# Kernel tuning notes

Hardware: AMD Instinct MI355X
Metric: run time of the kernel (lower is better)

Reference implementation:

```python
import jax, jax.numpy as jnp
import numpy as np

HID = 4544; NH = 71; NKV = 1; HD = 64  # Falcon-7B MQA geometry (head_dim hardcoded 64 in _split_heads)
B = 1; U = 32; C = 4; S = 2048          # batch, users, kv chunks, chunk length


def rotate_half(x):
    d = x.shape[-1] // 2
    return jnp.concatenate((-x[..., d:], x[..., :d]), axis=-1)


def setup_inputs() -> dict:
    key = jax.random.key(0)
    ks = jax.random.split(key, 7)
    hidden_states = jax.random.normal(ks[0], (B, U, HID), jnp.float32)
    cos = jax.random.uniform(ks[1], (1, U, 1, HD), jnp.float32, -1.0, 1.0)
    sin = jax.random.uniform(ks[2], (1, U, 1, HD), jnp.float32, -1.0, 1.0)
    k_cache = jax.random.normal(ks[3], (C, B, U, S, HD), jnp.float32)
    v_cache = jax.random.normal(ks[4], (C, B, U, S, HD), jnp.float32)
    attn_masks = jnp.zeros((C, B, U, S), jnp.float32)
    w_qkv = jax.random.normal(ks[5], ((NKV * (NH // NKV + 2)) * HD, HID), jnp.float32) * 0.02
    w_dense = jax.random.normal(ks[6], (HID, HID), jnp.float32) * 0.02
    return {"hidden_states": hidden_states, "cos": cos, "sin": sin,
            "k_cache": k_cache, "v_cache": v_cache, "attn_masks": attn_masks,
            "w_qkv": w_qkv, "w_dense": w_dense}


def reference(hidden_states, cos, sin, k_cache, v_cache, attn_masks, w_qkv, w_dense):
    b, u, _ = hidden_states.shape
    # fused QKV projection (Linear without bias: x @ W.T)
    fused = hidden_states @ w_qkv.T                      # [b,u,(NH+2*NKV)*HD]
    qkv = fused.reshape(b, u, NKV, NH // NKV + 2, HD)    # _split_heads view
    q = qkv[:, :, :, :-2].reshape(b, u, NH, HD)          # query heads
    k_cur = qkv[:, :, :, -2].reshape(b, u, NKV, HD)      # shared MQA key head
    v_cur = qkv[:, :, :, -1].reshape(b, u, NKV, HD)      # shared MQA value head
    # rotary embedding (apply_rotary_pos_emb)
    q = q * cos + rotate_half(q) * sin
    k_cur = k_cur * cos + rotate_half(k_cur) * sin
    inv = 1.0 / jnp.sqrt(jnp.float32(HD))
    # flash-decode over cached chunks: scores [c,b,u,n,s]
    scores = jnp.einsum('bund,cbusd->cbuns', q, k_cache) * inv
    scores = scores + attn_masks[:, :, :, None, :]
    m_c = jnp.max(scores, axis=-1, keepdims=True)        # [c,b,u,n,1] local max
    p = jnp.exp(scores - m_c)
    l_c = jnp.sum(p, axis=-1, keepdims=True)             # local row sums
    # current token = length-1 chunk (its local max is itself, local sum is 1)
    s_cur = jnp.einsum('bund,bued->bune', q, k_cur) * inv  # [b,u,n,1]
    g = jnp.maximum(jnp.max(m_c, axis=0), s_cur)           # global max [b,u,n,1]
    factor = jnp.exp(m_c - g[None])                        # per-chunk rescale
    out = jnp.einsum('cbuns,cbusd->bund', factor * p, v_cache)
    cur_w = jnp.exp(s_cur - g)                             # [b,u,n,1]
    out = out + cur_w * v_cur                              # v_cur broadcasts over heads
    scale = jnp.sum(factor * l_c, axis=0) + cur_w
    out = out / scale
    attn = out.reshape(b, u, NH * HD)
    return attn @ w_dense.T
```

## Files before the change

kernel.cpp:

```cpp
#include <hip/hip_runtime.h>
#include <hip/hip_bf16.h>

typedef __bf16 bf16_t;
typedef __bf16 bf16x8 __attribute__((ext_vector_type(8)));
typedef float  f32x4  __attribute__((ext_vector_type(4)));

#define MFMA16(A,B,C) __builtin_amdgcn_mfma_f32_16x16x32_bf16(A,B,C,0,0,0)

constexpr int HIDc = 4544;
constexpr int NHc  = 71;
constexpr int NHPc = 80;
constexpr int HDc  = 64;
constexpr int Uc   = 32;
constexpr int Sc   = 2048;
constexpr int RQ   = 4672;

constexpr size_t OFF_FUSED = 0;
constexpr size_t OFF_QHI   = 598016;
constexpr size_t OFF_QLO   = 925696;
constexpr size_t OFF_KCUR  = 1253376;
constexpr size_t OFF_VCUR  = 1261568;
constexpr size_t OFF_MP    = 1269760;
constexpr size_t OFF_LP    = 1415168;
constexpr size_t OFF_AHI   = 1560576;
constexpr size_t OFF_ALO   = 1851392;
constexpr size_t OFF_OP    = 2142208;

__device__ __forceinline__ bf16x8 ld8f(const float* base, long eidx) {
  const float* p = base + eidx;
  const f32x4 a = *(const f32x4*)p;
  const f32x4 b = *(const f32x4*)(p + 4);
  bf16x8 r;
  r[0]=(bf16_t)a[0]; r[1]=(bf16_t)a[1]; r[2]=(bf16_t)a[2]; r[3]=(bf16_t)a[3];
  r[4]=(bf16_t)b[0]; r[5]=(bf16_t)b[1]; r[6]=(bf16_t)b[2]; r[7]=(bf16_t)b[3];
  return r;
}

__device__ __forceinline__ void cp16(const float* g, float* l) {
  __builtin_amdgcn_global_load_lds((const __attribute__((address_space(1))) void*)g,
                                   (__attribute__((address_space(3))) void*)l, 16, 0, 0);
}
__device__ __forceinline__ void cp4(const float* g, float* l) {
  __builtin_amdgcn_global_load_lds((const __attribute__((address_space(1))) void*)g,
                                   (__attribute__((address_space(3))) void*)l, 4, 0, 0);
}

__global__ __launch_bounds__(256) void k_zeros(float* fused, float* out) {
  const int i = blockIdx.x*256 + threadIdx.x;
  if (i < Uc*RQ) fused[i] = 0.f;
  else           out[i - Uc*RQ] = 0.f;
}

__global__ __launch_bounds__(256) void k_qkv(
    const float* __restrict__ hidden, const float* __restrict__ wqkv,
    float* __restrict__ fused)
{
  const int h = blockIdx.x, y = blockIdx.y;
  const int t = threadIdx.x;
  const int wave = t >> 6, lane = t & 63;
  const int c = lane & 15, q4 = lane >> 4;
  const int mt = wave & 1, kh = wave >> 1;
  const int ks0 = y*18;
  const int ksn = min(18, 142 - ks0);
  const int h1  = ksn >> 1;
  const int kbeg = ks0 + (kh ? h1 : 0);
  const int kend = ks0 + (kh ? ksn : h1);
  __shared__ float sD[Uc*HDc];

  const long abase = (long)(mt*16 + c)*HIDc + q4*8;
  const long bbase = ((long)h*64 + c)*HIDc + q4*8;
  f32x4 acc[4] = {};
#pragma unroll 3
  for (int ks = kbeg; ks < kend; ++ks) {
    const bf16x8 af = ld8f(hidden, abase + ks*32);
#pragma unroll
    for (int nf = 0; nf < 4; ++nf) {
      const bf16x8 bv = ld8f(wqkv, bbase + (long)nf*16*HIDc + ks*32);
      acc[nf] = MFMA16(af, bv, acc[nf]);
    }
  }
  if (kh == 0) {
#pragma unroll
    for (int r = 0; r < 4; ++r)
#pragma unroll
      for (int nf = 0; nf < 4; ++nf)
        sD[(mt*16 + q4*4 + r)*64 + nf*16 + c] = acc[nf][r];
  }
  __syncthreads();
  if (kh == 1) {
#pragma unroll
    for (int r = 0; r < 4; ++r)
#pragma unroll
      for (int nf = 0; nf < 4; ++nf)
        sD[(mt*16 + q4*4 + r)*64 + nf*16 + c] += acc[nf][r];
  }
  __syncthreads();
  for (int i = t; i < Uc*HDc; i += 256)
    atomicAdd(&fused[(long)(i >> 6)*RQ + h*64 + (i & 63)], sD[i]);
}

__global__ __launch_bounds__(256) void k_rotary(
    const float* __restrict__ fused,
    const float* __restrict__ cosp, const float* __restrict__ sinp,
    bf16_t* __restrict__ qhi, bf16_t* __restrict__ qlo,
    float* __restrict__ kcur, float* __restrict__ vcur)
{
  const int h  = blockIdx.x;
  const int u0 = blockIdx.y*8;
  const int t = threadIdx.x;
  __shared__ float sD[8*HDc];
  if (h < 73) {
    for (int i = t; i < 8*HDc; i += 256)
      sD[i] = fused[(long)(u0 + (i >> 6))*RQ + h*64 + (i & 63)];
    __syncthreads();
  }
  if (h >= NHc) {
    for (int i = t; i < 8*HDc; i += 256) {
      const long idx = (((long)(u0 + (i >> 6)))*NHPc + h)*HDc + (i & 63);
      qhi[idx] = (bf16_t)0.f;  qlo[idx] = (bf16_t)0.f;
    }
  }
  if (h >= 73) return;
  for (int i = t; i < 8*HDc; i += 256) {
    const int u = u0 + (i >> 6), d = i & 63;
    const float x = sD[i];
    const float partner = sD[i ^ 32];
    const float cs = cosp[u*HDc + d];
    const float sn = sinp[u*HDc + d];
    const float rh = (d < 32) ? -partner : partner;
    const float val = x*cs + rh*sn;
    if (h < NHc) {
      const long idx = ((long)u*NHPc + h)*HDc + d;
      const bf16_t hi = (bf16_t)val;
      qhi[idx] = hi;
      qlo[idx] = (bf16_t)(val - (float)hi);
    } else if (h == NHc) {
      kcur[u*HDc + d] = val;
    } else {
      vcur[u*HDc + d] = x;
    }
  }
}

constexpr int ATTN_SLOT_F   = 4096;
constexpr int ATTN_STAGE_F  = 4*ATTN_SLOT_F;
constexpr int ATTN_SMEM_F   = ATTN_STAGE_F + 2048;
constexpr int ATTN_SMEM_BYTES = ATTN_SMEM_F * 4;

__global__ __launch_bounds__(512, 4) void k_attn(
    const float* __restrict__ kc, const float* __restrict__ vc,
    const float* __restrict__ masks,
    const bf16_t* __restrict__ qhi, const bf16_t* __restrict__ qlo,
    float* __restrict__ Mp, float* __restrict__ Lp, float* __restrict__ Op,
    const int NPB)
{
  extern __shared__ float smem[];
  const int u  = blockIdx.x;
  const int pb = blockIdx.y;
  const int tid = threadIdx.x;
  const int wave = __builtin_amdgcn_readfirstlane(tid >> 6);
  const int lane = tid & 63;
  const int c    = lane & 15;
  const int q4   = lane >> 4;
  const int pbpc = NPB >> 2;
  const int keys_pb = 2048 / pbpc;
  const int ph_cnt  = keys_pb >> 6;
  const int chunk = pb / pbpc;
  const int inner = pb - chunk*pbpc;
  const int s_base = inner*keys_pb;
  const long kvbase = ((long)(chunk*Uc + u))*Sc;

  float* const stage = smem;
  float* const smask = smem + ATTN_STAGE_F;

  const int srow = lane >> 4;
  const int scol = (lane & 15) << 2;

  if (wave >= 5) {
    if (wave == 7) {
      const int nmc = keys_pb >> 6;
      const float* gM = masks + kvbase + s_base;
      for (int i = 0; i < nmc; ++i)
        cp4(gM + i*64 + lane, smask + i*64);
      for (int p = 0; p < ph_cnt; ++p) {
        __builtin_amdgcn_s_barrier();
        if (p == 0) asm volatile("s_waitcnt vmcnt(0)" ::: "memory");
        __builtin_amdgcn_s_barrier();
      }
      return;
    }
    const float* gsrc = (wave == 5) ? kc : vc;
    const int vofs = (wave == 6) ? 2048 : 0;
#pragma unroll
    for (int sl = 0; sl < 2; ++sl) {
      const long tb = (kvbase + s_base + sl*32) * 64;
      float* dst = stage + sl*ATTN_SLOT_F + vofs;
#pragma unroll
      for (int i = 0; i < 8; ++i) {
        const int row = i*4 + srow;
        const int fz = ((row & 7) << 2) ^ (((row >> 3) & 1) << 4);
        cp16(gsrc + tb + row*64 + (scol ^ fz), dst + i*256);
      }
    }
    for (int p = 0; p < ph_cnt; ++p) {
      __builtin_amdgcn_s_barrier();
      if (p + 1 < ph_cnt) {
        const int g = ((p+1) & 1)*2;
#pragma unroll
        for (int sl = 0; sl < 2; ++sl) {
          const long tb = (kvbase + s_base + (long)(p+1)*64 + sl*32) * 64;
          float* dst = stage + (g + sl)*ATTN_SLOT_F + vofs;
#pragma unroll
          for (int i = 0; i < 8; ++i) {
            const int row = i*4 + srow;
            const int fz = ((row & 7) << 2) ^ (((row >> 3) & 1) << 4);
            cp16(gsrc + tb + row*64 + (scol ^ fz), dst + i*256);
          }
        }
        asm volatile("s_waitcnt vmcnt(16)" ::: "memory");
      } else {
        asm volatile("s_waitcnt vmcnt(0)" ::: "memory");
      }
      __builtin_amdgcn_s_barrier();
    }
    return;
  }

  const int ht = wave;
  bf16x8 qh[2], ql[2];
  {
    const bf16_t* qb  = qhi + ((long)u*NHPc + ht*16 + c)*HDc + q4*8;
    const bf16_t* qb2 = qlo + ((long)u*NHPc + ht*16 + c)*HDc + q4*8;
#pragma unroll
    for (int ks = 0; ks < 2; ++ks) {
      qh[ks] = *(const bf16x8*)(qb  + ks*32);
      ql[ks] = *(const bf16x8*)(qb2 + ks*32);
    }
  }

  float m_i = -INFINITY, l_i = 0.f;
  f32x4 Oa[4] = {};

  const int krow0 = ((c >> 2) << 3) + (c & 3);

  for (int p = 0; p < ph_cnt; ++p) {
    __syncthreads();
    __syncthreads();
    const int g = (p & 1)*2;

    f32x4 S[2][2];
    __builtin_amdgcn_s_setprio(1);
#pragma unroll
    for (int h2 = 0; h2 < 2; ++h2) {
      float* const lK = stage + (g + h2)*ATTN_SLOT_F;
#pragma unroll
      for (int mt2 = 0; mt2 < 2; ++mt2) {
        const int row = krow0 + mt2*4;
        const int fz = ((row & 7) << 2) ^ (((row >> 3) & 1) << 4);
        bf16x8 k0, k1;
#pragma unroll
        for (int ks = 0; ks < 2; ++ks) {
          const int b0 = row*64 + ((ks*32 + q4*8) ^ fz);
          const int b1 = row*64 + ((ks*32 + q4*8 + 4) ^ fz);
          const f32x4 a = *(const f32x4*)(lK + b0);
          const f32x4 b = *(const f32x4*)(lK + b1);
          bf16x8 r;
          r[0]=(bf16_t)a[0]; r[1]=(bf16_t)a[1]; r[2]=(bf16_t)a[2]; r[3]=(bf16_t)a[3];
          r[4]=(bf16_t)b[0]; r[5]=(bf16_t)b[1]; r[6]=(bf16_t)b[2]; r[7]=(bf16_t)b[3];
          if (ks == 0) k0 = r; else k1 = r;
        }
        f32x4 s = {};
        s = MFMA16(k0, qh[0], s);
        s = MFMA16(k1, qh[1], s);
        s = MFMA16(k0, ql[0], s);
        s = MFMA16(k1, ql[1], s);
        S[h2][mt2] = s;
      }
    }
    __builtin_amdgcn_s_setprio(0);

#pragma unroll
    for (int h2 = 0; h2 < 2; ++h2)
#pragma unroll
      for (int mt2 = 0; mt2 < 2; ++mt2)
#pragma unroll
        for (int r = 0; r < 4; ++r)
          S[h2][mt2][r] = S[h2][mt2][r]*0.125f
                        + smask[p*64 + h2*32 + q4*8 + mt2*4 + r];

    float tm = S[0][0][0];
#pragma unroll
    for (int h2 = 0; h2 < 2; ++h2)
#pragma unroll
      for (int mt2 = 0; mt2 < 2; ++mt2)
#pragma unroll
        for (int r = 0; r < 4; ++r) tm = fmaxf(tm, S[h2][mt2][r]);
    tm = fmaxf(tm, __shfl_xor(tm, 16));
    tm = fmaxf(tm, __shfl_xor(tm, 32));
    const float mn = fmaxf(m_i, tm);
    const float alpha = __expf(m_i - mn);
    m_i = mn;
#pragma unroll
    for (int h2 = 0; h2 < 2; ++h2)
#pragma unroll
      for (int mt2 = 0; mt2 < 2; ++mt2)
#pragma unroll
        for (int r = 0; r < 4; ++r)
          S[h2][mt2][r] = __expf(S[h2][mt2][r] - m_i);
    float rs = 0.f;
#pragma unroll
    for (int h2 = 0; h2 < 2; ++h2)
#pragma unroll
      for (int mt2 = 0; mt2 < 2; ++mt2)
#pragma unroll
        for (int r = 0; r < 4; ++r) rs += S[h2][mt2][r];
    rs += __shfl_xor(rs, 16);
    rs += __shfl_xor(rs, 32);
    l_i = l_i*alpha + rs;

#pragma unroll
    for (int r = 0; r < 4; ++r) {
      const float ar = __shfl(alpha, q4*4 + r);
#pragma unroll
      for (int dt = 0; dt < 4; ++dt) Oa[dt][r] *= ar;
    }

#pragma unroll
    for (int h2 = 0; h2 < 2; ++h2) {
      float* const lV = stage + (g + h2)*ATTN_SLOT_F + 2048;
      bf16x8 vf[4];
#pragma unroll
      for (int dt = 0; dt < 4; ++dt) {
        union { bf16_t e[8]; bf16x8 v; } uv;
#pragma unroll
        for (int j = 0; j < 8; ++j) {
          const int row = q4*8 + j;
          const int fz = ((row & 7) << 2) ^ (((row >> 3) & 1) << 4);
          uv.e[j] = (bf16_t)lV[row*64 + ((dt*16 + c) ^ fz)];
        }
        vf[dt] = uv.v;
      }
      bf16x8 ph, pl;
      {
        union { bf16_t e[8]; bf16x8 v; } uh, ul;
#pragma unroll
        for (int j = 0; j < 8; ++j) {
          const float val = (j < 4) ? S[h2][0][j] : S[h2][1][j & 3];
          const bf16_t hi = (bf16_t)val;
          uh.e[j] = hi;
          ul.e[j] = (bf16_t)(val - (float)hi);
        }
        ph = uh.v;  pl = ul.v;
      }
      __builtin_amdgcn_s_setprio(1);
#pragma unroll
      for (int dt = 0; dt < 4; ++dt) {
        Oa[dt] = MFMA16(ph, vf[dt], Oa[dt]);
        Oa[dt] = MFMA16(pl, vf[dt], Oa[dt]);
      }
      __builtin_amdgcn_s_setprio(0);
    }
  }

  float* op = Op + ((long)u*NPB + pb)*NHc*HDc;
#pragma unroll
  for (int dt = 0; dt < 4; ++dt)
#pragma unroll
    for (int r = 0; r < 4; ++r) {
      const int h = ht*16 + q4*4 + r;
      if (h < NHc) op[h*HDc + dt*16 + c] = Oa[dt][r];
    }
  if (q4 == 0) {
    const int hh = ht*16 + c;
    if (hh < NHc) {
      Mp[((long)u*NPB + pb)*NHc + hh] = fmaxf(m_i, -1e30f);
      Lp[((long)u*NPB + pb)*NHc + hh] = l_i;
    }
  }
}

__global__ __launch_bounds__(64) void k_combine(
    const float* __restrict__ Mp, const float* __restrict__ Lp,
    const float* __restrict__ Op,
    const bf16_t* __restrict__ qhi, const bf16_t* __restrict__ qlo,
    const float* __restrict__ kcur, const float* __restrict__ vcur,
    bf16_t* __restrict__ ahi, bf16_t* __restrict__ alo, const int NPB)
{
  const int h = blockIdx.x, u = blockIdx.y;
  const int lane = threadIdx.x;
  const long qidx = ((long)u*NHPc + h)*HDc + lane;
  float pr = ((float)qhi[qidx] + (float)qlo[qidx]) * kcur[u*HDc + lane];
#pragma unroll
  for (int o = 32; o > 0; o >>= 1) pr += __shfl_xor(pr, o);
  const float s_cur = pr * 0.125f;

  float g = s_cur;
  for (int p = 0; p < NPB; ++p)
    g = fmaxf(g, Mp[((long)u*NPB + p)*NHc + h]);
  g = fmaxf(g, -1e30f);
  float sw = 0.f, acc = 0.f;
  const float* ob = Op + (long)u*NPB*NHc*HDc + (long)h*HDc + lane;
  for (int p = 0; p < NPB; ++p) {
    const float f = __expf(Mp[((long)u*NPB + p)*NHc + h] - g);
    sw += f*Lp[((long)u*NPB + p)*NHc + h];
    acc += f*ob[(long)p*NHc*HDc];
  }
  const float cw = __expf(s_cur - g);
  acc += cw * vcur[u*HDc + lane];
  const float attn = acc / (sw + cw);
  const bf16_t hi = (bf16_t)attn;
  ahi[(long)u*HIDc + h*HDc + lane] = hi;
  alo[(long)u*HIDc + h*HDc + lane] = (bf16_t)(attn - (float)hi);
}

__global__ __launch_bounds__(256) void k_outgemm(
    const bf16_t* __restrict__ ahi, const bf16_t* __restrict__ alo,
    const float* __restrict__ wd, float* __restrict__ out)
{
  const int nb = blockIdx.x, y = blockIdx.y;
  const int t = threadIdx.x;
  const int wave = t >> 6, lane = t & 63;
  const int c = lane & 15, q4 = lane >> 4;
  const int mt = wave & 1, kh = wave >> 1;
  const int ks0 = y*18;
  const int ksn = min(18, 142 - ks0);
  const int h1  = ksn >> 1;
  const int kbeg = ks0 + (kh ? h1 : 0);
  const int kend = ks0 + (kh ? ksn : h1);
  __shared__ float sC[Uc*32];

  const bf16_t* aph = ahi + ((long)(mt*16 + c))*HIDc + q4*8;
  const bf16_t* apl = alo + ((long)(mt*16 + c))*HIDc + q4*8;
  const long bbase = ((long)nb*32 + c)*HIDc + q4*8;

  f32x4 acc[2] = {};
#pragma unroll 3
  for (int ks = kbeg; ks < kend; ++ks) {
    const bf16x8 Ah = *(const bf16x8*)(aph + ks*32);
    const bf16x8 Al = *(const bf16x8*)(apl + ks*32);
#pragma unroll
    for (int nf = 0; nf < 2; ++nf) {
      const bf16x8 B = ld8f(wd, bbase + (long)nf*16*HIDc + ks*32);
      acc[nf] = MFMA16(Ah, B, acc[nf]);
      acc[nf] = MFMA16(Al, B, acc[nf]);
    }
  }
  if (kh == 0) {
#pragma unroll
    for (int r = 0; r < 4; ++r)
#pragma unroll
      for (int nf = 0; nf < 2; ++nf)
        sC[(mt*16 + q4*4 + r)*32 + nf*16 + c] = acc[nf][r];
  }
  __syncthreads();
  if (kh == 1) {
#pragma unroll
    for (int r = 0; r < 4; ++r)
#pragma unroll
      for (int nf = 0; nf < 2; ++nf)
        sC[(mt*16 + q4*4 + r)*32 + nf*16 + c] += acc[nf][r];
  }
  __syncthreads();
  for (int i = t; i < Uc*32; i += 256)
    atomicAdd(&out[(long)(i >> 5)*HIDc + nb*32 + (i & 31)], sC[i]);
}

extern "C" void kernel_launch(void* const* d_in, const int* in_sizes, int n_in,
                              void* d_out, int out_size, void* d_ws, size_t ws_size,
                              hipStream_t stream)
{
  const float* hidden = (const float*)d_in[0];
  const float* cosp   = (const float*)d_in[1];
  const float* sinp   = (const float*)d_in[2];
  const float* kcache = (const float*)d_in[3];
  const float* vcache = (const float*)d_in[4];
  const float* masks  = (const float*)d_in[5];
  const float* wqkv   = (const float*)d_in[6];
  const float* wdense = (const float*)d_in[7];
  float* out = (float*)d_out;

  const size_t opb = (size_t)Uc*NHc*HDc*4;
  int NPB = 16;
  if      (ws_size >= OFF_OP + 16*opb) NPB = 16;
  else if (ws_size >= OFF_OP +  8*opb) NPB = 8;
  else if (ws_size >= OFF_OP +  4*opb) NPB = 4;
  else return;

  char* ws = (char*)d_ws;
  float*  fused = (float*)(ws + OFF_FUSED);
  bf16_t* qhi   = (bf16_t*)(ws + OFF_QHI);
  bf16_t* qlo   = (bf16_t*)(ws + OFF_QLO);
  float*  kcur  = (float*)(ws + OFF_KCUR);
  float*  vcur  = (float*)(ws + OFF_VCUR);
  float*  Mp    = (float*)(ws + OFF_MP);
  float*  Lp    = (float*)(ws + OFF_LP);
  bf16_t* ahi   = (bf16_t*)(ws + OFF_AHI);
  bf16_t* alo   = (bf16_t*)(ws + OFF_ALO);
  float*  Op    = (float*)(ws + OFF_OP);

  hipFuncSetAttribute(reinterpret_cast<const void*>(k_attn),
                      hipFuncAttributeMaxDynamicSharedMemorySize, ATTN_SMEM_BYTES);

  k_zeros  <<<1152, 256, 0, stream>>>(fused, out);
  k_qkv    <<<dim3(73, 8), 256, 0, stream>>>(hidden, wqkv, fused);
  k_rotary <<<dim3(80, 4), 256, 0, stream>>>(fused, cosp, sinp, qhi, qlo, kcur, vcur);
  k_attn   <<<dim3(32, NPB), 512, ATTN_SMEM_BYTES, stream>>>(kcache, vcache, masks, qhi, qlo, Mp, Lp, Op, NPB);
  k_combine<<<dim3(71, 32), 64, 0, stream>>>(Mp, Lp, Op, qhi, qlo, kcur, vcur, ahi, alo, NPB);
  k_outgemm<<<dim3(142, 8), 256, 0, stream>>>(ahi, alo, wdense, out);
}
```

Measured before the change: 337.8 us.

## Deepen attention KV prefetch ring to four stages and double GEMM split-K

The attention kernel's shared-memory staging changes from double buffering to a 4-slot ring, so producer waves prefetch three 64-key phases ahead with graded vmcnt waits. The aim is to hide HBM latency on the large fp32 K/V cache stream. In exchange, shared memory doubles, occupancy drops from 4 to 2 blocks per CU, and the attention grid shrinks from 16 to 8 partition blocks per user. The QKV and output GEMMs also split K into twice as many slices to raise parallelism, at the cost of more atomic adds.

```diff
diff --git a/kernel.cpp b/kernel.cpp
--- a/kernel.cpp
+++ b/kernel.cpp
@@ -60,8 +60,8 @@
   const int wave = t >> 6, lane = t & 63;
   const int c = lane & 15, q4 = lane >> 4;
   const int mt = wave & 1, kh = wave >> 1;
-  const int ks0 = y*18;
-  const int ksn = min(18, 142 - ks0);
+  const int ks0 = y*9;
+  const int ksn = min(9, 142 - ks0);
   const int h1  = ksn >> 1;
   const int kbeg = ks0 + (kh ? h1 : 0);
   const int kend = ks0 + (kh ? ksn : h1);
@@ -142,12 +142,13 @@
   }
 }
 
-constexpr int ATTN_SLOT_F   = 4096;
-constexpr int ATTN_STAGE_F  = 4*ATTN_SLOT_F;
+constexpr int ATTN_GRP_F    = 8192;
+constexpr int ATTN_RING     = 4;
+constexpr int ATTN_STAGE_F  = ATTN_RING*ATTN_GRP_F;
 constexpr int ATTN_SMEM_F   = ATTN_STAGE_F + 2048;
 constexpr int ATTN_SMEM_BYTES = ATTN_SMEM_F * 4;
 
-__global__ __launch_bounds__(512, 4) void k_attn(
+__global__ __launch_bounds__(512, 2) void k_attn(
     const float* __restrict__ kc, const float* __restrict__ vc,
     const float* __restrict__ masks,
     const bf16_t* __restrict__ qhi, const bf16_t* __restrict__ qlo,
@@ -190,26 +191,29 @@
       return;
     }
     const float* gsrc = (wave == 5) ? kc : vc;
-    const int vofs = (wave == 6) ? 2048 : 0;
-#pragma unroll
-    for (int sl = 0; sl < 2; ++sl) {
-      const long tb = (kvbase + s_base + sl*32) * 64;
-      float* dst = stage + sl*ATTN_SLOT_F + vofs;
-#pragma unroll
-      for (int i = 0; i < 8; ++i) {
-        const int row = i*4 + srow;
-        const int fz = ((row & 7) << 2) ^ (((row >> 3) & 1) << 4);
-        cp16(gsrc + tb + row*64 + (scol ^ fz), dst + i*256);
+    const int vofs = (wave == 6) ? 4096 : 0;
+#pragma unroll
+    for (int pt = 0; pt < 3; ++pt) {
+#pragma unroll
+      for (int sl = 0; sl < 2; ++sl) {
+        const long tb = (kvbase + s_base + pt*64 + sl*32) * 64;
+        float* dst = stage + pt*ATTN_GRP_F + vofs + sl*2048;
+#pragma unroll
+        for (int i = 0; i < 8; ++i) {
+          const int row = i*4 + srow;
+          const int fz = ((row & 7) << 2) ^ (((row >> 3) & 1) << 4);
+          cp16(gsrc + tb + row*64 + (scol ^ fz), dst + i*256);
+        }
       }
     }
     for (int p = 0; p < ph_cnt; ++p) {
       __builtin_amdgcn_s_barrier();
-      if (p + 1 < ph_cnt) {
-        const int g = ((p+1) & 1)*2;
+      if (p + 3 < ph_cnt) {
+        const int g = (p+3) & 3;
 #pragma unroll
         for (int sl = 0; sl < 2; ++sl) {
-          const long tb = (kvbase + s_base + (long)(p+1)*64 + sl*32) * 64;
-          float* dst = stage + (g + sl)*ATTN_SLOT_F + vofs;
+          const long tb = (kvbase + s_base + (long)(p+3)*64 + sl*32) * 64;
+          float* dst = stage + g*ATTN_GRP_F + vofs + sl*2048;
 #pragma unroll
           for (int i = 0; i < 8; ++i) {
             const int row = i*4 + srow;
@@ -217,10 +221,12 @@
             cp16(gsrc + tb + row*64 + (scol ^ fz), dst + i*256);
           }
         }
-        asm volatile("s_waitcnt vmcnt(16)" ::: "memory");
-      } else {
-        asm volatile("s_waitcnt vmcnt(0)" ::: "memory");
-      }
+      }
+      const int rem = min(3, ph_cnt - 1 - p);
+      if      (rem >= 3) asm volatile("s_waitcnt vmcnt(48)" ::: "memory");
+      else if (rem == 2) asm volatile("s_waitcnt vmcnt(32)" ::: "memory");
+      else if (rem == 1) asm volatile("s_waitcnt vmcnt(16)" ::: "memory");
+      else               asm volatile("s_waitcnt vmcnt(0)"  ::: "memory");
       __builtin_amdgcn_s_barrier();
     }
     return;
@@ -246,13 +252,13 @@
   for (int p = 0; p < ph_cnt; ++p) {
     __syncthreads();
     __syncthreads();
-    const int g = (p & 1)*2;
+    float* const grp = stage + (p & 3)*ATTN_GRP_F;
 
     f32x4 S[2][2];
     __builtin_amdgcn_s_setprio(1);
 #pragma unroll
     for (int h2 = 0; h2 < 2; ++h2) {
-      float* const lK = stage + (g + h2)*ATTN_SLOT_F;
+      float* const lK = grp + h2*2048;
 #pragma unroll
       for (int mt2 = 0; mt2 < 2; ++mt2) {
         const int row = krow0 + mt2*4;
@@ -327,7 +333,7 @@
 
 #pragma unroll
     for (int h2 = 0; h2 < 2; ++h2) {
-      float* const lV = stage + (g + h2)*ATTN_SLOT_F + 2048;
+      float* const lV = grp + 4096 + h2*2048;
       bf16x8 vf[4];
 #pragma unroll
       for (int dt = 0; dt < 4; ++dt) {
@@ -422,8 +428,8 @@
   const int wave = t >> 6, lane = t & 63;
   const int c = lane & 15, q4 = lane >> 4;
   const int mt = wave & 1, kh = wave >> 1;
-  const int ks0 = y*18;
-  const int ksn = min(18, 142 - ks0);
+  const int ks0 = y*9;
+  const int ksn = min(9, 142 - ks0);
   const int h1  = ksn >> 1;
   const int kbeg = ks0 + (kh ? h1 : 0);
   const int kend = ks0 + (kh ? ksn : h1);
@@ -480,10 +486,9 @@
   float* out = (float*)d_out;
 
   const size_t opb = (size_t)Uc*NHc*HDc*4;
-  int NPB = 16;
-  if      (ws_size >= OFF_OP + 16*opb) NPB = 16;
-  else if (ws_size >= OFF_OP +  8*opb) NPB = 8;
-  else if (ws_size >= OFF_OP +  4*opb) NPB = 4;
+  int NPB = 8;
+  if      (ws_size >= OFF_OP + 8*opb) NPB = 8;
+  else if (ws_size >= OFF_OP + 4*opb) NPB = 4;
   else return;
 
   char* ws = (char*)d_ws;
@@ -502,9 +507,9 @@
                       hipFuncAttributeMaxDynamicSharedMemorySize, ATTN_SMEM_BYTES);
 
   k_zeros  <<<1152, 256, 0, stream>>>(fused, out);
-  k_qkv    <<<dim3(73, 8), 256, 0, stream>>>(hidden, wqkv, fused);
+  k_qkv    <<<dim3(73, 16), 256, 0, stream>>>(hidden, wqkv, fused);
   k_rotary <<<dim3(80, 4), 256, 0, stream>>>(fused, cosp, sinp, qhi, qlo, kcur, vcur);
   k_attn   <<<dim3(32, NPB), 512, ATTN_SMEM_BYTES, stream>>>(kcache, vcache, masks, qhi, qlo, Mp, Lp, Op, NPB);
   k_combine<<<dim3(71, 32), 64, 0, stream>>>(Mp, Lp, Op, qhi, qlo, kcur, vcur, ahi, alo, NPB);
-  k_outgemm<<<dim3(142, 8), 256, 0, stream>>>(ahi, alo, wdense, out);
-}
+  k_outgemm<<<dim3(142, 16), 256, 0, stream>>>(ahi, alo, wdense, out);
+}
```

Result: faster. 325.0 us (-3.8%).
